# Kernel tuning notes

Hardware: AMD Instinct MI355X
Metric: run time of the kernel (lower is better)

Reference implementation:

```python
import jax, jax.numpy as jnp
import numpy as np

LN_EPS = 1e-5

def _layer_norm(y):
    # elementwise_affine=False LayerNorm over last dim
    mu = jnp.mean(y, axis=-1, keepdims=True)
    var = jnp.var(y, axis=-1, keepdims=True)
    return (y - mu) / jnp.sqrt(var + LN_EPS)

def setup_inputs() -> dict:
    key = jax.random.key(0)
    k0, k1, k2, k3, k4 = jax.random.split(key, 5)
    N, D, D_qk, D_v, n_out = 8192, 1024, 128, 1024, 1024
    w_std = 0.02
    x = jax.random.normal(k0, (N, D), dtype=jnp.float32)
    Wq = jax.random.normal(k1, (D_qk, D), dtype=jnp.float32) * w_std
    Wk = jax.random.normal(k2, (D_qk, D), dtype=jnp.float32) * w_std
    Wv = jax.random.normal(k3, (D_v, D), dtype=jnp.float32) * w_std
    Wl = jax.random.normal(k4, (n_out, D), dtype=jnp.float32) * w_std
    return {"x": x, "Wq": Wq, "Wk": Wk, "Wv": Wv, "Wl": Wl}

def reference(x, Wq, Wk, Wv, Wl):
    # Faithful to source: scores are MULTIPLIED by sqrt(D_qk) (the variable
    # dq_sqrt_inv is np.sqrt(D_qk), applied multiplicatively).
    scale = jnp.sqrt(jnp.asarray(Wq.shape[0], dtype=x.dtype))
    q = x @ Wq.T              # [N, D_qk]
    k = x @ Wk.T              # [N, D_qk]
    v = x @ Wv.T              # [N, D_v]
    attn = jax.nn.softmax(scale * (q @ k.T), axis=-1)  # [N, N]
    sa = attn @ v             # [N, D_v]
    h = _layer_norm(x + sa)   # residual + LN1
    return _layer_norm(sa + h @ Wl.T)  # linear + residual + LN2
```

## Files before the change

### kernel.cpp

```cpp
#include <hip/hip_runtime.h>
#include <hip/hip_bf16.h>
#include <math.h>

#define N_TOK 8192
#define D_IN  1024
#define D_QK  128

typedef short bf16x8 __attribute__((ext_vector_type(8)));
typedef float f32x4 __attribute__((ext_vector_type(4)));
typedef unsigned short u16;
typedef u16 u16x8 __attribute__((ext_vector_type(8)));

static __device__ __forceinline__ u16 f2bf(float f) {
  __hip_bfloat16 b = __float2bfloat16(f);
  return *(u16*)&b;
}
static __device__ __forceinline__ float bf2f(u16 u) {
  __hip_bfloat16 b = *(__hip_bfloat16*)&u;
  return __bfloat162float(b);
}

static __device__ __forceinline__ void gload_lds16(const void* g, void* lds) {
  __builtin_amdgcn_global_load_lds(
      (const __attribute__((address_space(1))) unsigned int*)g,
      (__attribute__((address_space(3))) unsigned int*)lds, 16, 0, 0);
}

template <int OUT_MODE>
__global__ __launch_bounds__(256, 2) void gemm_mfma(const u16* __restrict__ A,
                                                    const u16* __restrict__ B,
                                                    void* __restrict__ Cv,
                                                    int M, int N, int K) {
  __shared__ __align__(16) u16 As[128 * 32];
  __shared__ __align__(16) u16 Bs[128 * 32];
  const int tid = threadIdx.x;
  const int w = tid >> 6, l = tid & 63;
  const int lr = l & 15, lg = l >> 4;
  const int m0 = blockIdx.y * 128, n0 = blockIdx.x * 128;
  const int wr = (w >> 1) * 64, wc = (w & 1) * 64;

  f32x4 acc[4][4];
#pragma unroll
  for (int m = 0; m < 4; ++m)
#pragma unroll
    for (int n = 0; n < 4; ++n) {
      f32x4 z = {0.f, 0.f, 0.f, 0.f};
      acc[m][n] = z;
    }

  const int ldsb0 = (w * 2 + 0) * 1024;
  const int ldsb1 = (w * 2 + 1) * 1024;
  const int srow0 = (w * 2 + 0) * 16 + (l >> 2);
  const int srow1 = (w * 2 + 1) * 16 + (l >> 2);
  const int scol = (l & 3) * 8;

  for (int kt = 0; kt < K; kt += 32) {
    gload_lds16(A + (size_t)(m0 + srow0) * K + kt + scol, (char*)As + ldsb0);
    gload_lds16(A + (size_t)(m0 + srow1) * K + kt + scol, (char*)As + ldsb1);
    gload_lds16(B + (size_t)(n0 + srow0) * K + kt + scol, (char*)Bs + ldsb0);
    gload_lds16(B + (size_t)(n0 + srow1) * K + kt + scol, (char*)Bs + ldsb1);
    __syncthreads();
    bf16x8 af[4], bfr[4];
#pragma unroll
    for (int m = 0; m < 4; ++m)
      af[m] = *(const bf16x8*)((char*)As + (wr + m * 16 + lr) * 64 + lg * 16);
#pragma unroll
    for (int n = 0; n < 4; ++n)
      bfr[n] = *(const bf16x8*)((char*)Bs + (wc + n * 16 + lr) * 64 + lg * 16);
#pragma unroll
    for (int m = 0; m < 4; ++m)
#pragma unroll
      for (int n = 0; n < 4; ++n)
        acc[m][n] = __builtin_amdgcn_mfma_f32_16x16x32_bf16(af[m], bfr[n], acc[m][n], 0, 0, 0);
    __syncthreads();
  }
#pragma unroll
  for (int m = 0; m < 4; ++m)
#pragma unroll
    for (int n = 0; n < 4; ++n)
#pragma unroll
      for (int r = 0; r < 4; ++r) {
        const int row = m0 + wr + m * 16 + lg * 4 + r;
        const int col = n0 + wc + n * 16 + lr;
        if (OUT_MODE == 1) {
          ((float*)Cv)[(size_t)row * N + col] = acc[m][n][r];
        } else if (OUT_MODE == 0) {
          ((u16*)Cv)[(size_t)row * N + col] = f2bf(acc[m][n][r]);
        } else {
          const size_t adr = ((size_t)(row >> 4) * 256 + (col >> 5)) * 512 +
                             ((row & 15) + (((col >> 3) & 3) << 4)) * 8 + (col & 7);
          ((u16*)Cv)[adr] = f2bf(acc[m][n][r]);
        }
      }
}

__global__ __launch_bounds__(256, 2) void gemm_hilo(
    const u16* __restrict__ Ah, const u16* __restrict__ Al,
    const u16* __restrict__ BhQ, const u16* __restrict__ BlQ,
    u16* __restrict__ ChQ, u16* __restrict__ ClQ,
    const u16* __restrict__ BhK, const u16* __restrict__ BlK,
    u16* __restrict__ ChK, u16* __restrict__ ClK, int K) {
  const bool isQ = (blockIdx.x == 0);
  const u16* Bh = isQ ? BhQ : BhK;
  const u16* Bl = isQ ? BlQ : BlK;
  u16* Ch = isQ ? ChQ : ChK;
  u16* Cl = isQ ? ClQ : ClK;
  const float scale = isQ ? 11.31370849898476f : 1.0f;
  __shared__ __align__(16) u16 Ahs[64 * 32], Als[64 * 32];
  __shared__ __align__(16) u16 Bhs[128 * 32], Bls[128 * 32];
  const int tid = threadIdx.x;
  const int w = tid >> 6, l = tid & 63;
  const int lr = l & 15, lg = l >> 4;
  const int m0 = blockIdx.y * 64;
  const int wc = w * 32;

  f32x4 acc[4][2];
#pragma unroll
  for (int m = 0; m < 4; ++m)
#pragma unroll
    for (int n = 0; n < 2; ++n) {
      f32x4 z = {0.f, 0.f, 0.f, 0.f};
      acc[m][n] = z;
    }

  const int arow = w * 16 + (l >> 2);
  const int brow0 = (w * 2 + 0) * 16 + (l >> 2);
  const int brow1 = (w * 2 + 1) * 16 + (l >> 2);
  const int scol = (l & 3) * 8;

  for (int kt = 0; kt < K; kt += 32) {
    gload_lds16(Ah + (size_t)(m0 + arow) * K + kt + scol, (char*)Ahs + w * 1024);
    gload_lds16(Al + (size_t)(m0 + arow) * K + kt + scol, (char*)Als + w * 1024);
    gload_lds16(Bh + (size_t)brow0 * K + kt + scol, (char*)Bhs + (w * 2 + 0) * 1024);
    gload_lds16(Bh + (size_t)brow1 * K + kt + scol, (char*)Bhs + (w * 2 + 1) * 1024);
    gload_lds16(Bl + (size_t)brow0 * K + kt + scol, (char*)Bls + (w * 2 + 0) * 1024);
    gload_lds16(Bl + (size_t)brow1 * K + kt + scol, (char*)Bls + (w * 2 + 1) * 1024);
    __syncthreads();
    bf16x8 afh[4], afl[4], bfh[2], bfl[2];
#pragma unroll
    for (int m = 0; m < 4; ++m) {
      afh[m] = *(const bf16x8*)((char*)Ahs + (m * 16 + lr) * 64 + lg * 16);
      afl[m] = *(const bf16x8*)((char*)Als + (m * 16 + lr) * 64 + lg * 16);
    }
#pragma unroll
    for (int n = 0; n < 2; ++n) {
      bfh[n] = *(const bf16x8*)((char*)Bhs + (wc + n * 16 + lr) * 64 + lg * 16);
      bfl[n] = *(const bf16x8*)((char*)Bls + (wc + n * 16 + lr) * 64 + lg * 16);
    }
#pragma unroll
    for (int m = 0; m < 4; ++m)
#pragma unroll
      for (int n = 0; n < 2; ++n) {
        acc[m][n] = __builtin_amdgcn_mfma_f32_16x16x32_bf16(afh[m], bfh[n], acc[m][n], 0, 0, 0);
        acc[m][n] = __builtin_amdgcn_mfma_f32_16x16x32_bf16(afh[m], bfl[n], acc[m][n], 0, 0, 0);
        acc[m][n] = __builtin_amdgcn_mfma_f32_16x16x32_bf16(afl[m], bfh[n], acc[m][n], 0, 0, 0);
      }
    __syncthreads();
  }
#pragma unroll
  for (int m = 0; m < 4; ++m)
#pragma unroll
    for (int n = 0; n < 2; ++n)
#pragma unroll
      for (int r = 0; r < 4; ++r) {
        const size_t row = m0 + m * 16 + lg * 4 + r;
        const size_t col = wc + n * 16 + lr;
        const float v = acc[m][n][r] * scale;
        const u16 h = f2bf(v);
        Ch[row * 128 + col] = h;
        Cl[row * 128 + col] = f2bf(v - bf2f(h));
      }
}

__global__ __launch_bounds__(256) void cvt_bf16(const float* __restrict__ in,
                                                u16* __restrict__ out) {
  const size_t idx = (size_t)blockIdx.x * 256 + threadIdx.x;
  const float4 a = ((const float4*)in)[idx * 2];
  const float4 b = ((const float4*)in)[idx * 2 + 1];
  u16x8 o;
  o[0] = f2bf(a.x); o[1] = f2bf(a.y); o[2] = f2bf(a.z); o[3] = f2bf(a.w);
  o[4] = f2bf(b.x); o[5] = f2bf(b.y); o[6] = f2bf(b.z); o[7] = f2bf(b.w);
  ((u16x8*)out)[idx] = o;
}

__global__ __launch_bounds__(256) void split_hl(const float* __restrict__ in,
                                                u16* __restrict__ hi,
                                                u16* __restrict__ lo) {
  const size_t idx = (size_t)blockIdx.x * 256 + threadIdx.x;
  const float4 v = ((const float4*)in)[idx];
  float f[4] = {v.x, v.y, v.z, v.w};
  u16 h[4], g[4];
#pragma unroll
  for (int i = 0; i < 4; ++i) {
    h[i] = f2bf(f[i]);
    g[i] = f2bf(f[i] - bf2f(h[i]));
  }
  ushort4 hv; hv.x = h[0]; hv.y = h[1]; hv.z = h[2]; hv.w = h[3];
  ushort4 gv; gv.x = g[0]; gv.y = g[1]; gv.z = g[2]; gv.w = g[3];
  ((ushort4*)hi)[idx] = hv;
  ((ushort4*)lo)[idx] = gv;
}

__global__ __launch_bounds__(256) void repack_k(const u16* __restrict__ krh,
                                                const u16* __restrict__ krl,
                                                u16* __restrict__ khT,
                                                u16* __restrict__ klT) {
  const int gid = blockIdx.x * 256 + threadIdx.x;
  const int f = gid >> 6, l = gid & 63;
  const int fn = f >> 2, fk = f & 3;
  const size_t src = (size_t)(fn * 16 + (l & 15)) * 128 + fk * 32 + (l >> 4) * 8;
  *(u16x8*)(khT + (size_t)f * 512 + l * 8) = *(const u16x8*)(krh + src);
  *(u16x8*)(klT + (size_t)f * 512 + l * 8) = *(const u16x8*)(krl + src);
}

__global__ __launch_bounds__(512) __attribute__((amdgpu_waves_per_eu(2, 4)))
void flash_attn_mfma(const u16* __restrict__ qh, const u16* __restrict__ ql,
                     const u16* __restrict__ khT, const u16* __restrict__ klT,
                     const u16* __restrict__ vt, float* __restrict__ sa) {
  __shared__ __align__(16) u16 Qs[2 * 8192];
  __shared__ __align__(16) u16 P[64 * 128];
  __shared__ __align__(16) float pmax[64][12];
  __shared__ __align__(16) float lpart[64][12];
  __shared__ __align__(16) float facl[64];
  const int tid = threadIdx.x;
  const int w = tid >> 6, l = tid & 63;
  const int lr = l & 15, lg = l >> 4;
  const int q0 = blockIdx.y * 64;
  const int half = blockIdx.x;

  {
#pragma unroll
    for (int i = 0; i < 2; ++i) {
      const int e = i * 512 + tid;
      const int row = e >> 4, c16 = e & 15;
      const u16x8 hv = *(const u16x8*)(qh + (size_t)(q0 + row) * 128 + c16 * 8);
      const u16x8 lv = *(const u16x8*)(ql + (size_t)(q0 + row) * 128 + c16 * 8);
      const int b = (row * 256 + c16 * 16) ^ ((row & 7) << 4);
      *(u16x8*)((char*)Qs + b) = hv;
      *(u16x8*)((char*)Qs + 16384 + b) = lv;
    }
  }

  float mrun4[4] = {-INFINITY, -INFINITY, -INFINITY, -INFINITY};
  float lrun4[4] = {0.f, 0.f, 0.f, 0.f};

  f32x4 acc[4][4];
#pragma unroll
  for (int mt = 0; mt < 4; ++mt)
#pragma unroll
    for (int nt = 0; nt < 4; ++nt) {
      f32x4 z = {0.f, 0.f, 0.f, 0.f};
      acc[mt][nt] = z;
    }

  bf16x8 kfh[4], kfl[4];
#pragma unroll
  for (int ks = 0; ks < 4; ++ks) {
    kfh[ks] = *(const bf16x8*)(khT + ((size_t)w * 4 + ks) * 512 + l * 8);
    kfl[ks] = *(const bf16x8*)(klT + ((size_t)w * 4 + ks) * 512 + l * 8);
  }
  __syncthreads();

  const int vcol0 = half * 32 + w * 4;

  for (int t = 0; t < 64; ++t) {
    const int c = t * 4;
    f32x4 sfT[4];
#pragma unroll
    for (int mt = 0; mt < 4; ++mt) {
      f32x4 z = {0.f, 0.f, 0.f, 0.f};
      sfT[mt] = z;
    }
    __builtin_amdgcn_s_setprio(1);
#pragma unroll
    for (int ks = 0; ks < 4; ++ks)
#pragma unroll
      for (int mt = 0; mt < 4; ++mt) {
        const int b = ((mt * 16 + lr) * 256 + ks * 64 + lg * 16) ^ ((lr & 7) << 4);
        const bf16x8 qfh = *(const bf16x8*)((char*)Qs + b);
        const bf16x8 qfl = *(const bf16x8*)((char*)Qs + 16384 + b);
        sfT[mt] = __builtin_amdgcn_mfma_f32_16x16x32_bf16(kfh[ks], qfh, sfT[mt], 0, 0, 0);
        sfT[mt] = __builtin_amdgcn_mfma_f32_16x16x32_bf16(kfl[ks], qfh, sfT[mt], 0, 0, 0);
        sfT[mt] = __builtin_amdgcn_mfma_f32_16x16x32_bf16(kfh[ks], qfl, sfT[mt], 0, 0, 0);
      }
    __builtin_amdgcn_s_setprio(0);
    if (t < 63) {
#pragma unroll
      for (int ks = 0; ks < 4; ++ks) {
        kfh[ks] = *(const bf16x8*)(khT + ((size_t)((t + 1) * 8 + w) * 4 + ks) * 512 + l * 8);
        kfl[ks] = *(const bf16x8*)(klT + ((size_t)((t + 1) * 8 + w) * 4 + ks) * 512 + l * 8);
      }
    }
    bf16x8 vA[4], vB[4];
#pragma unroll
    for (int nt = 0; nt < 4; ++nt)
      vA[nt] = *(const bf16x8*)(vt + ((size_t)(vcol0 + nt) * 256 + c + 0) * 512 + l * 8);

    float wmax[4];
#pragma unroll
    for (int mt = 0; mt < 4; ++mt)
      wmax[mt] = fmaxf(fmaxf(sfT[mt][0], sfT[mt][1]), fmaxf(sfT[mt][2], sfT[mt][3]));
#pragma unroll
    for (int mt = 0; mt < 4; ++mt) {
      wmax[mt] = fmaxf(wmax[mt], __shfl_xor(wmax[mt], 16));
      wmax[mt] = fmaxf(wmax[mt], __shfl_xor(wmax[mt], 32));
    }
    if (lg == 0) {
#pragma unroll
      for (int mt = 0; mt < 4; ++mt) pmax[mt * 16 + lr][w] = wmax[mt];
    }
    __syncthreads();

    float mn4[4], fac4[4];
#pragma unroll
    for (int mt = 0; mt < 4; ++mt) {
      const int q = mt * 16 + lr;
      const f32x4 a = *(const f32x4*)&pmax[q][0];
      const f32x4 b = *(const f32x4*)&pmax[q][4];
      const float mx = fmaxf(fmaxf(fmaxf(a[0], a[1]), fmaxf(a[2], a[3])),
                             fmaxf(fmaxf(b[0], b[1]), fmaxf(b[2], b[3])));
      const float mn = fmaxf(mrun4[mt], mx);
      fac4[mt] = __expf(mrun4[mt] - mn);
      mn4[mt] = mn;
      mrun4[mt] = mn;
    }
    if (w == 0 && lg == 0) {
#pragma unroll
      for (int mt = 0; mt < 4; ++mt) facl[mt * 16 + lr] = fac4[mt];
    }
#pragma unroll
    for (int mt = 0; mt < 4; ++mt) {
      const float e0 = __expf(sfT[mt][0] - mn4[mt]);
      const float e1 = __expf(sfT[mt][1] - mn4[mt]);
      const float e2 = __expf(sfT[mt][2] - mn4[mt]);
      const float e3 = __expf(sfT[mt][3] - mn4[mt]);
      float tot = (e0 + e1) + (e2 + e3);
      tot += __shfl_xor(tot, 16);
      tot += __shfl_xor(tot, 32);
      lrun4[mt] = lrun4[mt] * fac4[mt] + tot;
      ushort4 pb;
      pb.x = f2bf(e0); pb.y = f2bf(e1); pb.z = f2bf(e2); pb.w = f2bf(e3);
      const int q = mt * 16 + lr;
      const int byte = (q * 256 + w * 32 + lg * 8) ^ ((q & 7) << 4);
      *(ushort4*)((char*)P + byte) = pb;
    }
    __syncthreads();

#pragma unroll
    for (int mt = 0; mt < 4; ++mt) {
      const f32x4 f4 = *(const f32x4*)&facl[mt * 16 + lg * 4];
#pragma unroll
      for (int rr = 0; rr < 4; ++rr) {
        const float f = f4[rr];
        if (f != 1.0f) {
#pragma unroll
          for (int nt = 0; nt < 4; ++nt) acc[mt][nt][rr] *= f;
        }
      }
    }

#pragma unroll
    for (int ks = 0; ks < 4; ++ks) {
      bf16x8* nxt = (ks & 1) ? vA : vB;
      if (ks < 3) {
#pragma unroll
        for (int nt = 0; nt < 4; ++nt)
          nxt[nt] = *(const bf16x8*)(vt + ((size_t)(vcol0 + nt) * 256 + c + ks + 1) * 512 + l * 8);
      }
      const bf16x8* cur = (ks & 1) ? vB : vA;
      bf16x8 pf[4];
#pragma unroll
      for (int mt = 0; mt < 4; ++mt) {
        const int row = mt * 16 + lr;
        pf[mt] = *(const bf16x8*)((char*)P + ((row * 256 + ks * 64 + lg * 16) ^ ((row & 7) << 4)));
      }
      __builtin_amdgcn_s_setprio(1);
#pragma unroll
      for (int mt = 0; mt < 4; ++mt)
#pragma unroll
        for (int nt = 0; nt < 4; ++nt)
          acc[mt][nt] = __builtin_amdgcn_mfma_f32_16x16x32_bf16(pf[mt], cur[nt], acc[mt][nt], 0, 0, 0);
      __builtin_amdgcn_s_setprio(0);
    }
  }
  if (lg == 0) {
#pragma unroll
    for (int mt = 0; mt < 4; ++mt) lpart[mt * 16 + lr][w] = lrun4[mt];
  }
  __syncthreads();
#pragma unroll
  for (int mt = 0; mt < 4; ++mt)
#pragma unroll
    for (int rr = 0; rr < 4; ++rr) {
      const int row = mt * 16 + lg * 4 + rr;
      const f32x4 a = *(const f32x4*)&lpart[row][0];
      const f32x4 b = *(const f32x4*)&lpart[row][4];
      const float inv =
          1.0f / (((a[0] + a[1]) + (a[2] + a[3])) + ((b[0] + b[1]) + (b[2] + b[3])));
#pragma unroll
      for (int nt = 0; nt < 4; ++nt)
        sa[(size_t)(q0 + row) * 1024 + half * 512 + w * 64 + nt * 16 + lr] =
            acc[mt][nt][rr] * inv;
    }
}

__global__ __launch_bounds__(256) void ln_add(const float* __restrict__ a,
                                              const float* __restrict__ b,
                                              float* __restrict__ o) {
  const int row = blockIdx.x;
  const int tid = threadIdx.x;
  const size_t base = (size_t)row * 256 + tid;
  const float4 av = ((const float4*)a)[base];
  const float4 bv = ((const float4*)b)[base];
  float4 y;
  y.x = av.x + bv.x; y.y = av.y + bv.y;
  y.z = av.z + bv.z; y.w = av.w + bv.w;
  float s1 = y.x + y.y + y.z + y.w;
  float s2 = y.x * y.x + y.y * y.y + y.z * y.z + y.w * y.w;
#pragma unroll
  for (int off = 32; off > 0; off >>= 1) {
    s1 += __shfl_xor(s1, off);
    s2 += __shfl_xor(s2, off);
  }
  __shared__ float r1[4];
  __shared__ float r2[4];
  if ((tid & 63) == 0) { r1[tid >> 6] = s1; r2[tid >> 6] = s2; }
  __syncthreads();
  s1 = r1[0] + r1[1] + r1[2] + r1[3];
  s2 = r2[0] + r2[1] + r2[2] + r2[3];
  const float mu = s1 * (1.0f / 1024.0f);
  const float var = s2 * (1.0f / 1024.0f) - mu * mu;
  const float rs = rsqrtf(var + 1e-5f);
  float4 ov;
  ov.x = (y.x - mu) * rs; ov.y = (y.y - mu) * rs;
  ov.z = (y.z - mu) * rs; ov.w = (y.w - mu) * rs;
  ((float4*)o)[base] = ov;
}

__global__ __launch_bounds__(256) void ln_add_bf16(const float* __restrict__ a,
                                                   const float* __restrict__ b,
                                                   u16* __restrict__ o) {
  const int row = blockIdx.x;
  const int tid = threadIdx.x;
  const size_t base = (size_t)row * 256 + tid;
  const float4 av = ((const float4*)a)[base];
  const float4 bv = ((const float4*)b)[base];
  float4 y;
  y.x = av.x + bv.x; y.y = av.y + bv.y;
  y.z = av.z + bv.z; y.w = av.w + bv.w;
  float s1 = y.x + y.y + y.z + y.w;
  float s2 = y.x * y.x + y.y * y.y + y.z * y.z + y.w * y.w;
#pragma unroll
  for (int off = 32; off > 0; off >>= 1) {
    s1 += __shfl_xor(s1, off);
    s2 += __shfl_xor(s2, off);
  }
  __shared__ float r1[4];
  __shared__ float r2[4];
  if ((tid & 63) == 0) { r1[tid >> 6] = s1; r2[tid >> 6] = s2; }
  __syncthreads();
  s1 = r1[0] + r1[1] + r1[2] + r1[3];
  s2 = r2[0] + r2[1] + r2[2] + r2[3];
  const float mu = s1 * (1.0f / 1024.0f);
  const float var = s2 * (1.0f / 1024.0f) - mu * mu;
  const float rs = rsqrtf(var + 1e-5f);
  ushort4 ov;
  ov.x = f2bf((y.x - mu) * rs); ov.y = f2bf((y.y - mu) * rs);
  ov.z = f2bf((y.z - mu) * rs); ov.w = f2bf((y.w - mu) * rs);
  ((ushort4*)o)[base] = ov;
}

extern "C" void kernel_launch(void* const* d_in, const int* in_sizes, int n_in,
                              void* d_out, int out_size, void* d_ws, size_t ws_size,
                              hipStream_t stream) {
  const float* x  = (const float*)d_in[0];
  const float* Wq = (const float*)d_in[1];
  const float* Wk = (const float*)d_in[2];
  const float* Wv = (const float*)d_in[3];
  const float* Wl = (const float*)d_in[4];
  float* out = (float*)d_out;

  char* w8 = (char*)d_ws;
  u16* xh  = (u16*)(w8 + (0ull << 20));
  u16* xl  = (u16*)(w8 + (16ull << 20));
  u16* khT = (u16*)(w8 + (16ull << 20));
  u16* klT = (u16*)(w8 + (18ull << 20));
  u16* qh  = (u16*)(w8 + (32ull << 20));
  u16* ql  = (u16*)(w8 + (34ull << 20));
  u16* krh = (u16*)(w8 + (36ull << 20));
  u16* krl = (u16*)(w8 + (38ull << 20));
  u16* hb  = (u16*)(w8 + (32ull << 20));
  u16* vtt = (u16*)(w8 + (48ull << 20));
  float* sa = (float*)(w8 + (64ull << 20));
  u16* wqh = (u16*)(w8 + (92ull << 20));
  u16* wql = (u16*)(w8 + (92ull << 20) + (256ull << 10));
  u16* wkh = (u16*)(w8 + (92ull << 20) + (512ull << 10));
  u16* wkl = (u16*)(w8 + (92ull << 20) + (768ull << 10));
  u16* Wvb = (u16*)(w8 + (96ull << 20));
  u16* Wlb = (u16*)(w8 + (98ull << 20));

  split_hl<<<8192, 256, 0, stream>>>(x, xh, xl);
  cvt_bf16<<<512, 256, 0, stream>>>(Wv, Wvb);
  cvt_bf16<<<512, 256, 0, stream>>>(Wl, Wlb);
  gemm_mfma<2><<<dim3(64, 8), 256, 0, stream>>>(Wvb, xh, (void*)vtt, D_IN, N_TOK, D_IN);
  split_hl<<<128, 256, 0, stream>>>(Wq, wqh, wql);
  split_hl<<<128, 256, 0, stream>>>(Wk, wkh, wkl);
  gemm_hilo<<<dim3(2, 128), 256, 0, stream>>>(xh, xl, wqh, wql, qh, ql,
                                              wkh, wkl, krh, krl, D_IN);
  repack_k<<<512, 256, 0, stream>>>(krh, krl, khT, klT);
  flash_attn_mfma<<<dim3(2, 128), 512, 0, stream>>>(qh, ql, khT, klT, vtt, sa);
  ln_add_bf16<<<N_TOK, 256, 0, stream>>>(x, sa, hb);
  gemm_mfma<1><<<dim3(8, 64), 256, 0, stream>>>(hb, Wlb, (void*)out, N_TOK, D_IN, D_IN);
  ln_add<<<N_TOK, 256, 0, stream>>>(sa, out, out);
}
```

Measured before the change: 418.7 us.

## Split flash attention over key halves and merge partials in fused combine+LN kernel

Adds a split-K dimension to the flash attention grid so each block processes half of the key sequence, doubling the block count from 256 to 512 to better fill the GPU's CUs. Partial outputs are stored as bf16 along with per-row max and sum. A new combine kernel rescales and merges them, then applies the residual LayerNorm. The sa intermediate becomes bf16 for the final LN. This adds extra partial-output traffic and bf16 rounding of unnormalized partials, which risks precision loss.

New measurement: 418.9 us. About the same (+0.0%).

```diff
diff --git a/kernel.cpp b/kernel.cpp
--- a/kernel.cpp
+++ b/kernel.cpp
@@ -216,7 +216,8 @@
 __global__ __launch_bounds__(512) __attribute__((amdgpu_waves_per_eu(2, 4)))
 void flash_attn_mfma(const u16* __restrict__ qh, const u16* __restrict__ ql,
                      const u16* __restrict__ khT, const u16* __restrict__ klT,
-                     const u16* __restrict__ vt, float* __restrict__ sa) {
+                     const u16* __restrict__ vt, u16* __restrict__ part,
+                     float* __restrict__ mfin, float* __restrict__ lfin) {
   __shared__ __align__(16) u16 Qs[2 * 8192];
   __shared__ __align__(16) u16 P[64 * 128];
   __shared__ __align__(16) float pmax[64][12];
@@ -227,6 +228,8 @@
   const int lr = l & 15, lg = l >> 4;
   const int q0 = blockIdx.y * 64;
   const int half = blockIdx.x;
+  const int z = blockIdx.z;
+  const int tbase = z * 32;
 
   {
 #pragma unroll
@@ -249,27 +252,28 @@
   for (int mt = 0; mt < 4; ++mt)
 #pragma unroll
     for (int nt = 0; nt < 4; ++nt) {
-      f32x4 z = {0.f, 0.f, 0.f, 0.f};
-      acc[mt][nt] = z;
+      f32x4 z4 = {0.f, 0.f, 0.f, 0.f};
+      acc[mt][nt] = z4;
     }
 
   bf16x8 kfh[4], kfl[4];
 #pragma unroll
   for (int ks = 0; ks < 4; ++ks) {
-    kfh[ks] = *(const bf16x8*)(khT + ((size_t)w * 4 + ks) * 512 + l * 8);
-    kfl[ks] = *(const bf16x8*)(klT + ((size_t)w * 4 + ks) * 512 + l * 8);
+    kfh[ks] = *(const bf16x8*)(khT + ((size_t)(tbase * 8 + w) * 4 + ks) * 512 + l * 8);
+    kfl[ks] = *(const bf16x8*)(klT + ((size_t)(tbase * 8 + w) * 4 + ks) * 512 + l * 8);
   }
   __syncthreads();
 
   const int vcol0 = half * 32 + w * 4;
 
-  for (int t = 0; t < 64; ++t) {
+  for (int tt = 0; tt < 32; ++tt) {
+    const int t = tbase + tt;
     const int c = t * 4;
     f32x4 sfT[4];
 #pragma unroll
     for (int mt = 0; mt < 4; ++mt) {
-      f32x4 z = {0.f, 0.f, 0.f, 0.f};
-      sfT[mt] = z;
+      f32x4 z4 = {0.f, 0.f, 0.f, 0.f};
+      sfT[mt] = z4;
     }
     __builtin_amdgcn_s_setprio(1);
 #pragma unroll
@@ -284,7 +288,7 @@
         sfT[mt] = __builtin_amdgcn_mfma_f32_16x16x32_bf16(kfh[ks], qfl, sfT[mt], 0, 0, 0);
       }
     __builtin_amdgcn_s_setprio(0);
-    if (t < 63) {
+    if (tt < 31) {
 #pragma unroll
       for (int ks = 0; ks < 4; ++ks) {
         kfh[ks] = *(const bf16x8*)(khT + ((size_t)((t + 1) * 8 + w) * 4 + ks) * 512 + l * 8);
@@ -387,7 +391,13 @@
 #pragma unroll
     for (int mt = 0; mt < 4; ++mt) lpart[mt * 16 + lr][w] = lrun4[mt];
   }
+  if (w == 0 && lg == 0) {
+#pragma unroll
+    for (int mt = 0; mt < 4; ++mt)
+      mfin[(size_t)z * N_TOK + q0 + mt * 16 + lr] = mrun4[mt];
+  }
   __syncthreads();
+  u16* pz = part + (size_t)z * N_TOK * D_IN;
 #pragma unroll
   for (int mt = 0; mt < 4; ++mt)
 #pragma unroll
@@ -395,26 +405,75 @@
       const int row = mt * 16 + lg * 4 + rr;
       const f32x4 a = *(const f32x4*)&lpart[row][0];
       const f32x4 b = *(const f32x4*)&lpart[row][4];
-      const float inv =
-          1.0f / (((a[0] + a[1]) + (a[2] + a[3])) + ((b[0] + b[1]) + (b[2] + b[3])));
+      const float lsum =
+          ((a[0] + a[1]) + (a[2] + a[3])) + ((b[0] + b[1]) + (b[2] + b[3]));
+      if (w == 0 && lr == 0) lfin[(size_t)z * N_TOK + q0 + row] = lsum;
 #pragma unroll
       for (int nt = 0; nt < 4; ++nt)
-        sa[(size_t)(q0 + row) * 1024 + half * 512 + w * 64 + nt * 16 + lr] =
-            acc[mt][nt][rr] * inv;
-    }
-}
-
-__global__ __launch_bounds__(256) void ln_add(const float* __restrict__ a,
-                                              const float* __restrict__ b,
-                                              float* __restrict__ o) {
+        pz[(size_t)(q0 + row) * 1024 + half * 512 + w * 64 + nt * 16 + lr] =
+            f2bf(acc[mt][nt][rr]);
+    }
+}
+
+__global__ __launch_bounds__(256) void comb_ln(const u16* __restrict__ part,
+                                               const float* __restrict__ mfin,
+                                               const float* __restrict__ lfin,
+                                               const float* __restrict__ x,
+                                               u16* __restrict__ sa_bf,
+                                               u16* __restrict__ hb) {
   const int row = blockIdx.x;
   const int tid = threadIdx.x;
   const size_t base = (size_t)row * 256 + tid;
-  const float4 av = ((const float4*)a)[base];
-  const float4 bv = ((const float4*)b)[base];
+  const float m0 = mfin[row], m1 = mfin[N_TOK + row];
+  const float l0 = lfin[row], l1 = lfin[N_TOK + row];
+  const float m = fmaxf(m0, m1);
+  const float a0 = __expf(m0 - m), a1 = __expf(m1 - m);
+  const float inv = 1.0f / (a0 * l0 + a1 * l1);
+  const float s0 = a0 * inv, s1 = a1 * inv;
+  const ushort4 p0 = ((const ushort4*)part)[base];
+  const ushort4 p1 = ((const ushort4*)(part + (size_t)N_TOK * D_IN))[base];
+  float o0 = s0 * bf2f(p0.x) + s1 * bf2f(p1.x);
+  float o1 = s0 * bf2f(p0.y) + s1 * bf2f(p1.y);
+  float o2 = s0 * bf2f(p0.z) + s1 * bf2f(p1.z);
+  float o3 = s0 * bf2f(p0.w) + s1 * bf2f(p1.w);
+  ushort4 sv;
+  sv.x = f2bf(o0); sv.y = f2bf(o1); sv.z = f2bf(o2); sv.w = f2bf(o3);
+  ((ushort4*)sa_bf)[base] = sv;
+  const float4 xv = ((const float4*)x)[base];
   float4 y;
-  y.x = av.x + bv.x; y.y = av.y + bv.y;
-  y.z = av.z + bv.z; y.w = av.w + bv.w;
+  y.x = xv.x + o0; y.y = xv.y + o1; y.z = xv.z + o2; y.w = xv.w + o3;
+  float s1r = y.x + y.y + y.z + y.w;
+  float s2r = y.x * y.x + y.y * y.y + y.z * y.z + y.w * y.w;
+#pragma unroll
+  for (int off = 32; off > 0; off >>= 1) {
+    s1r += __shfl_xor(s1r, off);
+    s2r += __shfl_xor(s2r, off);
+  }
+  __shared__ float r1[4];
+  __shared__ float r2[4];
+  if ((tid & 63) == 0) { r1[tid >> 6] = s1r; r2[tid >> 6] = s2r; }
+  __syncthreads();
+  s1r = r1[0] + r1[1] + r1[2] + r1[3];
+  s2r = r2[0] + r2[1] + r2[2] + r2[3];
+  const float mu = s1r * (1.0f / 1024.0f);
+  const float var = s2r * (1.0f / 1024.0f) - mu * mu;
+  const float rs = rsqrtf(var + 1e-5f);
+  ushort4 ov;
+  ov.x = f2bf((y.x - mu) * rs); ov.y = f2bf((y.y - mu) * rs);
+  ov.z = f2bf((y.z - mu) * rs); ov.w = f2bf((y.w - mu) * rs);
+  ((ushort4*)hb)[base] = ov;
+}
+
+__global__ __launch_bounds__(256) void ln_final(const u16* __restrict__ sa_bf,
+                                                float* __restrict__ o) {
+  const int row = blockIdx.x;
+  const int tid = threadIdx.x;
+  const size_t base = (size_t)row * 256 + tid;
+  const ushort4 sv = ((const ushort4*)sa_bf)[base];
+  const float4 ov = ((const float4*)o)[base];
+  float4 y;
+  y.x = ov.x + bf2f(sv.x); y.y = ov.y + bf2f(sv.y);
+  y.z = ov.z + bf2f(sv.z); y.w = ov.w + bf2f(sv.w);
   float s1 = y.x + y.y + y.z + y.w;
   float s2 = y.x * y.x + y.y * y.y + y.z * y.z + y.w * y.w;
 #pragma unroll
@@ -431,43 +490,10 @@
   const float mu = s1 * (1.0f / 1024.0f);
   const float var = s2 * (1.0f / 1024.0f) - mu * mu;
   const float rs = rsqrtf(var + 1e-5f);
-  float4 ov;
-  ov.x = (y.x - mu) * rs; ov.y = (y.y - mu) * rs;
-  ov.z = (y.z - mu) * rs; ov.w = (y.w - mu) * rs;
-  ((float4*)o)[base] = ov;
-}
-
-__global__ __launch_bounds__(256) void ln_add_bf16(const float* __restrict__ a,
-                                                   const float* __restrict__ b,
-                                                   u16* __restrict__ o) {
-  const int row = blockIdx.x;
-  const int tid = threadIdx.x;
-  const size_t base = (size_t)row * 256 + tid;
-  const float4 av = ((const float4*)a)[base];
-  const float4 bv = ((const float4*)b)[base];
-  float4 y;
-  y.x = av.x + bv.x; y.y = av.y + bv.y;
-  y.z = av.z + bv.z; y.w = av.w + bv.w;
-  float s1 = y.x + y.y + y.z + y.w;
-  float s2 = y.x * y.x + y.y * y.y + y.z * y.z + y.w * y.w;
-#pragma unroll
-  for (int off = 32; off > 0; off >>= 1) {
-    s1 += __shfl_xor(s1, off);
-    s2 += __shfl_xor(s2, off);
-  }
-  __shared__ float r1[4];
-  __shared__ float r2[4];
-  if ((tid & 63) == 0) { r1[tid >> 6] = s1; r2[tid >> 6] = s2; }
-  __syncthreads();
-  s1 = r1[0] + r1[1] + r1[2] + r1[3];
-  s2 = r2[0] + r2[1] + r2[2] + r2[3];
-  const float mu = s1 * (1.0f / 1024.0f);
-  const float var = s2 * (1.0f / 1024.0f) - mu * mu;
-  const float rs = rsqrtf(var + 1e-5f);
-  ushort4 ov;
-  ov.x = f2bf((y.x - mu) * rs); ov.y = f2bf((y.y - mu) * rs);
-  ov.z = f2bf((y.z - mu) * rs); ov.w = f2bf((y.w - mu) * rs);
-  ((ushort4*)o)[base] = ov;
+  float4 res;
+  res.x = (y.x - mu) * rs; res.y = (y.y - mu) * rs;
+  res.z = (y.z - mu) * rs; res.w = (y.w - mu) * rs;
+  ((float4*)o)[base] = res;
 }
 
 extern "C" void kernel_launch(void* const* d_in, const int* in_sizes, int n_in,
@@ -481,21 +507,24 @@
   float* out = (float*)d_out;
 
   char* w8 = (char*)d_ws;
-  u16* xh  = (u16*)(w8 + (0ull << 20));
-  u16* xl  = (u16*)(w8 + (16ull << 20));
-  u16* khT = (u16*)(w8 + (16ull << 20));
-  u16* klT = (u16*)(w8 + (18ull << 20));
-  u16* qh  = (u16*)(w8 + (32ull << 20));
-  u16* ql  = (u16*)(w8 + (34ull << 20));
-  u16* krh = (u16*)(w8 + (36ull << 20));
-  u16* krl = (u16*)(w8 + (38ull << 20));
-  u16* hb  = (u16*)(w8 + (32ull << 20));
-  u16* vtt = (u16*)(w8 + (48ull << 20));
-  float* sa = (float*)(w8 + (64ull << 20));
-  u16* wqh = (u16*)(w8 + (92ull << 20));
-  u16* wql = (u16*)(w8 + (92ull << 20) + (256ull << 10));
-  u16* wkh = (u16*)(w8 + (92ull << 20) + (512ull << 10));
-  u16* wkl = (u16*)(w8 + (92ull << 20) + (768ull << 10));
+  u16* xh    = (u16*)(w8 + (0ull << 20));
+  u16* xl    = (u16*)(w8 + (16ull << 20));
+  u16* khT   = (u16*)(w8 + (16ull << 20));
+  u16* klT   = (u16*)(w8 + (18ull << 20));
+  u16* sa_bf = (u16*)(w8 + (0ull << 20));
+  u16* hb    = (u16*)(w8 + (20ull << 20));
+  u16* qh    = (u16*)(w8 + (32ull << 20));
+  u16* ql    = (u16*)(w8 + (34ull << 20));
+  u16* krh   = (u16*)(w8 + (36ull << 20));
+  u16* krl   = (u16*)(w8 + (38ull << 20));
+  float* mfin = (float*)(w8 + (36ull << 20));
+  float* lfin = (float*)(w8 + (36ull << 20) + (128ull << 10));
+  u16* wqh = (u16*)(w8 + (40ull << 20));
+  u16* wql = (u16*)(w8 + (40ull << 20) + (256ull << 10));
+  u16* wkh = (u16*)(w8 + (40ull << 20) + (512ull << 10));
+  u16* wkl = (u16*)(w8 + (40ull << 20) + (768ull << 10));
+  u16* vtt   = (u16*)(w8 + (48ull << 20));
+  u16* part  = (u16*)(w8 + (64ull << 20));
   u16* Wvb = (u16*)(w8 + (96ull << 20));
   u16* Wlb = (u16*)(w8 + (98ull << 20));
 
@@ -508,8 +537,9 @@
   gemm_hilo<<<dim3(2, 128), 256, 0, stream>>>(xh, xl, wqh, wql, qh, ql,
                                               wkh, wkl, krh, krl, D_IN);
   repack_k<<<512, 256, 0, stream>>>(krh, krl, khT, klT);
-  flash_attn_mfma<<<dim3(2, 128), 512, 0, stream>>>(qh, ql, khT, klT, vtt, sa);
-  ln_add_bf16<<<N_TOK, 256, 0, stream>>>(x, sa, hb);
+  flash_attn_mfma<<<dim3(2, 128, 2), 512, 0, stream>>>(qh, ql, khT, klT, vtt,
+                                                       part, mfin, lfin);
+  comb_ln<<<N_TOK, 256, 0, stream>>>(part, mfin, lfin, x, sa_bf, hb);
   gemm_mfma<1><<<dim3(8, 64), 256, 0, stream>>>(hb, Wlb, (void*)out, N_TOK, D_IN, D_IN);
-  ln_add<<<N_TOK, 256, 0, stream>>>(sa, out, out);
-}
+  ln_final<<<N_TOK, 256, 0, stream>>>(sa_bf, out);
+}
```
